# Kernel optimization log

Measured on AMD Instinct MI355X. Metric: run time of the kernel, lower is better.

The kernel has to match this reference:

```python
import jax, jax.numpy as jnp
import numpy as np

N_NODES, N_EDGES, N_GRAPHS = 500000, 2000000, 16384


def _lin(key, fan_in, fan_out):
    # torch nn.Linear default init: U(-1/sqrt(fan_in), 1/sqrt(fan_in))
    s = 1.0 / np.sqrt(fan_in)
    kw, kb = jax.random.split(key)
    W = jax.random.uniform(kw, (fan_in, fan_out), jnp.float32, -s, s)
    b = jax.random.uniform(kb, (fan_out,), jnp.float32, -s, s)
    return W, b


def setup_inputs() -> dict:
    key = jax.random.key(0)
    ks = jax.random.split(key, 16)
    x = jax.random.normal(ks[0], (N_NODES, 131), jnp.float32)
    edge_src = jax.random.randint(ks[1], (N_EDGES,), 0, N_NODES, jnp.int32)
    edge_dst = jax.random.randint(ks[2], (N_EDGES,), 0, N_NODES, jnp.int32)
    batch_index = jnp.sort(jax.random.randint(ks[3], (N_NODES,), 0, N_GRAPHS, jnp.int32))
    solvent_descriptors = jax.random.normal(ks[4], (N_GRAPHS, 11), jnp.float32)
    Wc1, bc1 = _lin(ks[5], 131, 128)
    Wc2, bc2 = _lin(ks[6], 128, 64)
    W1, b1 = _lin(ks[7], 64 + 11, 2048)
    W2, b2 = _lin(ks[8], 2048, 1024)
    W3, b3 = _lin(ks[9], 1024, 128)
    # 6 property heads, stacked: Linear(128,32) -> ReLU -> Linear(32,1)
    Wh1 = jnp.stack([_lin(jax.random.fold_in(ks[10], i), 128, 32)[0] for i in range(6)])
    bh1 = jnp.stack([_lin(jax.random.fold_in(ks[10], i), 128, 32)[1] for i in range(6)])
    Wh2 = jnp.stack([_lin(jax.random.fold_in(ks[11], i), 32, 1)[0] for i in range(6)])
    bh2 = jnp.stack([_lin(jax.random.fold_in(ks[11], i), 32, 1)[1] for i in range(6)])
    return dict(x=x, edge_src=edge_src, edge_dst=edge_dst, batch_index=batch_index,
                solvent_descriptors=solvent_descriptors,
                Wc1=Wc1, bc1=bc1, Wc2=Wc2, bc2=bc2,
                W1=W1, b1=b1, W2=W2, b2=b2, W3=W3, b3=b3,
                Wh1=Wh1, bh1=bh1, Wh2=Wh2, bh2=bh2,
                num_graphs=N_GRAPHS)


def _gcn_conv(x, W, b, src, dst, n_nodes):
    # PyG GCNConv: add self-loops, symmetric normalization, scatter-add aggregate.
    h = x @ W                                           # [N, F_out]
    deg = jnp.zeros((n_nodes,), x.dtype).at[dst].add(1.0) + 1.0  # +1 for self-loop
    dinv = jax.lax.rsqrt(deg)                            # deg >= 1
    norm = dinv[src] * dinv[dst]                         # [E]
    agg = jnp.zeros_like(h).at[dst].add(norm[:, None] * h[src])
    agg = agg + h * (dinv * dinv)[:, None]               # self-loop contribution
    return agg + b


def reference(x, edge_src, edge_dst, batch_index, solvent_descriptors,
              Wc1, bc1, Wc2, bc2, W1, b1, W2, b2, W3, b3,
              Wh1, bh1, Wh2, bh2, num_graphs):
    n = x.shape[0]
    h = jax.nn.relu(_gcn_conv(x, Wc1, bc1, edge_src, edge_dst, n))
    h = _gcn_conv(h, Wc2, bc2, edge_src, edge_dst, n)
    g = jax.ops.segment_sum(h, batch_index, num_segments=num_graphs)  # global sum pool [G,64]
    z = jnp.concatenate([g, solvent_descriptors], axis=1)             # [G,75]
    z = jax.nn.relu(z @ W1 + b1)   # dropout is identity in eval
    z = jax.nn.relu(z @ W2 + b2)
    z = jax.nn.relu(z @ W3 + b3)   # [G,128]
    a = jax.nn.relu(jnp.einsum('gf,hfk->ghk', z, Wh1) + bh1)          # [G,6,32]
    out = jnp.einsum('ghk,hk->gh', a, Wh2[..., 0]) + bh2[:, 0]        # [G,6]
    return out
```

## Files before the change

kernel.cpp:

```cpp
#include <hip/hip_runtime.h>

#define N_NODES 500000
#define N_EDGES 2000000
#define N_GRAPHS 16384
#define STRIP 16

#define SCAN_ELEMS 2048
#define SCAN_NBLK ((N_NODES + SCAN_ELEMS - 1) / SCAN_ELEMS)

typedef short bf16x8 __attribute__((ext_vector_type(8)));
typedef float f32x4 __attribute__((ext_vector_type(4)));
typedef unsigned short u16x8 __attribute__((ext_vector_type(8)));

__device__ __forceinline__ unsigned short f2bf_rne(float x) {
    unsigned int b = __float_as_uint(x);
    unsigned int r = (b + 0x7fffu + ((b >> 16) & 1u)) >> 16;
    return (unsigned short)r;
}
__device__ __forceinline__ float bf2f(unsigned short h) {
    return __uint_as_float(((unsigned int)h) << 16);
}
__device__ __forceinline__ void split_bf(float v, unsigned short& hi, unsigned short& lo) {
    hi = f2bf_rne(v);
    lo = f2bf_rne(v - bf2f(hi));
}

__global__ __launch_bounds__(256) void k_zero_counts(int* counts) {
    int i = blockIdx.x * 256 + threadIdx.x;
    if (i < N_NODES) counts[i] = 0;
}
__global__ __launch_bounds__(256) void k_hist(const int* __restrict__ dst, int* __restrict__ counts) {
    int e = blockIdx.x * 256 + threadIdx.x;
    if (e < N_EDGES) atomicAdd(&counts[dst[e]], 1);
}
__global__ __launch_bounds__(256) void k_scan_reduce(const int* __restrict__ counts, int* __restrict__ bsum) {
    int b = blockIdx.x, t = threadIdx.x;
    int base_i = b * SCAN_ELEMS + t * 8;
    int s = 0;
    #pragma unroll
    for (int j = 0; j < 8; j++) { int i = base_i + j; if (i < N_NODES) s += counts[i]; }
    __shared__ int sh[256];
    sh[t] = s; __syncthreads();
    for (int off = 128; off > 0; off >>= 1) { if (t < off) sh[t] += sh[t + off]; __syncthreads(); }
    if (t == 0) bsum[b] = sh[0];
}
__global__ __launch_bounds__(256) void k_scan_bsum(const int* __restrict__ bsum, int* __restrict__ boff,
                                                   int* __restrict__ row_ptr) {
    __shared__ int sh[256];
    int t = threadIdx.x;
    int v = (t < SCAN_NBLK) ? bsum[t] : 0;
    sh[t] = v; __syncthreads();
    for (int off = 1; off < 256; off <<= 1) {
        int u = (t >= off) ? sh[t - off] : 0;
        __syncthreads();
        sh[t] += u; __syncthreads();
    }
    boff[t] = sh[t] - v;
    if (t == 255) row_ptr[N_NODES] = sh[255];
}
__global__ __launch_bounds__(256) void k_scan_final(const int* __restrict__ counts, const int* __restrict__ boff,
                                                    int* __restrict__ row_ptr, int* __restrict__ cursor,
                                                    float* __restrict__ dinv) {
    __shared__ int sh[256];
    int b = blockIdx.x, t = threadIdx.x;
    int base_i = b * SCAN_ELEMS + t * 8;
    int c[8]; int tsum = 0;
    #pragma unroll
    for (int j = 0; j < 8; j++) {
        int i = base_i + j;
        c[j] = (i < N_NODES) ? counts[i] : 0;
        tsum += c[j];
    }
    sh[t] = tsum; __syncthreads();
    for (int off = 1; off < 256; off <<= 1) {
        int u = (t >= off) ? sh[t - off] : 0;
        __syncthreads();
        sh[t] += u; __syncthreads();
    }
    int run = boff[b] + sh[t] - tsum;
    #pragma unroll
    for (int j = 0; j < 8; j++) {
        int i = base_i + j;
        if (i < N_NODES) {
            row_ptr[i] = run;
            cursor[i]  = run;
            dinv[i]    = rsqrtf((float)c[j] + 1.0f);
        }
        run += c[j];
    }
}
__global__ __launch_bounds__(256) void k_fill(const int* __restrict__ esrc, const int* __restrict__ edst,
                                              int* __restrict__ cursor, int* __restrict__ srcs) {
    int e = blockIdx.x * 256 + threadIdx.x;
    if (e >= N_EDGES) return;
    int d = edst[e];
    int pos = atomicAdd(&cursor[d], 1);
    srcs[pos] = esrc[e];
}
__global__ __launch_bounds__(256) void k_gstart(const int* __restrict__ batch, int* __restrict__ gstart) {
    int g = blockIdx.x * 256 + threadIdx.x;
    if (g > N_GRAPHS) return;
    if (g == N_GRAPHS) { gstart[g] = N_NODES; return; }
    int lo = 0, hi = N_NODES;
    while (lo < hi) { int mid = (lo + hi) >> 1; if (batch[mid] < g) lo = mid + 1; else hi = mid; }
    gstart[g] = lo;
}
__global__ __launch_bounds__(256) void k_zero_P(float* P) {
    int i = blockIdx.x * 256 + threadIdx.x;
    if (i < N_GRAPHS * 128) P[i] = 0.0f;
}

template<int KTOT>
__global__ __launch_bounds__(256) void k_gemm_conv1(const float* __restrict__ A,
                                                    const float* __restrict__ B,
                                                    unsigned short* __restrict__ C, int Mreal) {
    __shared__ float As[8][132];
    __shared__ float Bs[8][132];
    const int tid = threadIdx.x;
    const int bm = blockIdx.x;
    const int tr = (tid >> 4) << 3;
    const int tc = (tid & 15) << 3;
    float acc[8][8] = {};
    const int la_r = tid >> 1, la_c = (tid & 1) << 2;
    const int lb_r = tid >> 5, lb_c = (tid & 31) << 2;
    const int arow = min(bm * 128 + la_r, Mreal - 1);
    const float* Ap = A + (size_t)arow * KTOT + la_c;
    constexpr int KMAIN = (KTOT / 8) * 8;
    for (int k0 = 0; k0 < KMAIN; k0 += 8) {
        float4 a4 = *(const float4*)(Ap + k0);
        float4 b4 = *(const float4*)(B + (size_t)(k0 + lb_r) * 128 + lb_c);
        __syncthreads();
        As[la_c + 0][la_r] = a4.x;
        As[la_c + 1][la_r] = a4.y;
        As[la_c + 2][la_r] = a4.z;
        As[la_c + 3][la_r] = a4.w;
        *(float4*)&Bs[lb_r][lb_c] = b4;
        __syncthreads();
        #pragma unroll
        for (int k = 0; k < 8; k++) {
            float a[8], b[8];
            *(float4*)&a[0] = *(const float4*)&As[k][tr];
            *(float4*)&a[4] = *(const float4*)&As[k][tr + 4];
            *(float4*)&b[0] = *(const float4*)&Bs[k][tc];
            *(float4*)&b[4] = *(const float4*)&Bs[k][tc + 4];
            #pragma unroll
            for (int i = 0; i < 8; i++)
                #pragma unroll
                for (int j = 0; j < 8; j++)
                    acc[i][j] = fmaf(a[i], b[j], acc[i][j]);
        }
    }
    if (KTOT % 8 != 0) {
        constexpr int k0 = KMAIN;
        float av[4];
        #pragma unroll
        for (int j = 0; j < 4; j++) av[j] = (k0 + la_c + j < KTOT) ? Ap[k0 + j] : 0.0f;
        float4 b4 = {0.f, 0.f, 0.f, 0.f};
        if (k0 + lb_r < KTOT) b4 = *(const float4*)(B + (size_t)(k0 + lb_r) * 128 + lb_c);
        __syncthreads();
        As[la_c + 0][la_r] = av[0];
        As[la_c + 1][la_r] = av[1];
        As[la_c + 2][la_r] = av[2];
        As[la_c + 3][la_r] = av[3];
        *(float4*)&Bs[lb_r][lb_c] = b4;
        __syncthreads();
        #pragma unroll
        for (int k = 0; k < 8; k++) {
            float a[8], b[8];
            *(float4*)&a[0] = *(const float4*)&As[k][tr];
            *(float4*)&a[4] = *(const float4*)&As[k][tr + 4];
            *(float4*)&b[0] = *(const float4*)&Bs[k][tc];
            *(float4*)&b[4] = *(const float4*)&Bs[k][tc + 4];
            #pragma unroll
            for (int i = 0; i < 8; i++)
                #pragma unroll
                for (int j = 0; j < 8; j++)
                    acc[i][j] = fmaf(a[i], b[j], acc[i][j]);
        }
    }
    const int row0 = bm * 128 + tr;
    #pragma unroll
    for (int i = 0; i < 8; i++) {
        if (row0 + i < Mreal) {
            u16x8 o;
            #pragma unroll
            for (int j = 0; j < 8; j++) o[j] = f2bf_rne(acc[i][j]);
            *(u16x8*)(C + (size_t)(row0 + i) * 128 + tc) = o;
        }
    }
}

__global__ __launch_bounds__(256) void k_gather1(const unsigned short* __restrict__ h,
                                                 const float* __restrict__ dinv,
                                                 const float* __restrict__ bias,
                                                 const int* __restrict__ row_ptr, const int* __restrict__ srcs,
                                                 unsigned short* __restrict__ r1) {
    int g = blockIdx.x * 256 + threadIdx.x;
    int n = g >> 6, lane = g & 63;
    if (n >= N_NODES) return;
    float dn = dinv[n];
    int c = lane * 2;
    unsigned int hv = *(const unsigned int*)(h + (size_t)n * 128 + c);
    float s2 = dn * dn;
    float a0 = fmaf(s2, bf2f((unsigned short)(hv & 0xffffu)), bias[c]);
    float a1 = fmaf(s2, bf2f((unsigned short)(hv >> 16)), bias[c + 1]);
    int e0 = row_ptr[n], e1 = row_ptr[n + 1];
    int e = e0;
    for (; e + 2 <= e1; e += 2) {
        int sA = srcs[e], sB = srcs[e + 1];
        float nA = dinv[sA] * dn, nB = dinv[sB] * dn;
        unsigned int hA = *(const unsigned int*)(h + (size_t)sA * 128 + c);
        unsigned int hB = *(const unsigned int*)(h + (size_t)sB * 128 + c);
        a0 = fmaf(nA, bf2f((unsigned short)(hA & 0xffffu)), a0);
        a1 = fmaf(nA, bf2f((unsigned short)(hA >> 16)), a1);
        a0 = fmaf(nB, bf2f((unsigned short)(hB & 0xffffu)), a0);
        a1 = fmaf(nB, bf2f((unsigned short)(hB >> 16)), a1);
    }
    if (e < e1) {
        int sA = srcs[e];
        float nA = dinv[sA] * dn;
        unsigned int hA = *(const unsigned int*)(h + (size_t)sA * 128 + c);
        a0 = fmaf(nA, bf2f((unsigned short)(hA & 0xffffu)), a0);
        a1 = fmaf(nA, bf2f((unsigned short)(hA >> 16)), a1);
    }
    a0 = fmaxf(a0, 0.0f);
    a1 = fmaxf(a1, 0.0f);
    unsigned int o = (unsigned int)f2bf_rne(a0) | ((unsigned int)f2bf_rne(a1) << 16);
    *(unsigned int*)(r1 + (size_t)n * 128 + c) = o;
}

__global__ __launch_bounds__(256) void k_g2p(const unsigned short* __restrict__ r1,
                                             const float* __restrict__ dinv,
                                             const int* __restrict__ row_ptr, const int* __restrict__ srcs,
                                             const int* __restrict__ batch,
                                             float* __restrict__ P) {
    int gw = (blockIdx.x * 256 + threadIdx.x) >> 6;
    int lane = threadIdx.x & 63;
    if (gw >= N_NODES / STRIP) return;
    int n0 = gw * STRIP;
    int c = lane * 2;
    float a0 = 0.0f, a1 = 0.0f;
    int cur_g = batch[n0];
    for (int n = n0; n < n0 + STRIP; n++) {
        int bg = batch[n];
        if (bg != cur_g) {
            atomicAdd(&P[(size_t)cur_g * 128 + c], a0);
            atomicAdd(&P[(size_t)cur_g * 128 + c + 1], a1);
            a0 = a1 = 0.0f;
            cur_g = bg;
        }
        float dn = dinv[n];
        float s2 = dn * dn;
        unsigned int hv = *(const unsigned int*)(r1 + (size_t)n * 128 + c);
        a0 = fmaf(s2, bf2f((unsigned short)(hv & 0xffffu)), a0);
        a1 = fmaf(s2, bf2f((unsigned short)(hv >> 16)), a1);
        int e0 = row_ptr[n], e1 = row_ptr[n + 1];
        int e = e0;
        for (; e + 2 <= e1; e += 2) {
            int sA = srcs[e], sB = srcs[e + 1];
            float nA = dinv[sA] * dn, nB = dinv[sB] * dn;
            unsigned int hA = *(const unsigned int*)(r1 + (size_t)sA * 128 + c);
            unsigned int hB = *(const unsigned int*)(r1 + (size_t)sB * 128 + c);
            a0 = fmaf(nA, bf2f((unsigned short)(hA & 0xffffu)), a0);
            a1 = fmaf(nA, bf2f((unsigned short)(hA >> 16)), a1);
            a0 = fmaf(nB, bf2f((unsigned short)(hB & 0xffffu)), a0);
            a1 = fmaf(nB, bf2f((unsigned short)(hB >> 16)), a1);
        }
        if (e < e1) {
            int sA = srcs[e];
            float nA = dinv[sA] * dn;
            unsigned int hA = *(const unsigned int*)(r1 + (size_t)sA * 128 + c);
            a0 = fmaf(nA, bf2f((unsigned short)(hA & 0xffffu)), a0);
            a1 = fmaf(nA, bf2f((unsigned short)(hA >> 16)), a1);
        }
    }
    atomicAdd(&P[(size_t)cur_g * 128 + c], a0);
    atomicAdd(&P[(size_t)cur_g * 128 + c + 1], a1);
}

__global__ __launch_bounds__(128) void k_zg(const float* __restrict__ P, const int* __restrict__ gstart,
                                            const float* __restrict__ Wc2, const float* __restrict__ bc2,
                                            const float* __restrict__ solv, float* __restrict__ zpad) {
    int g = blockIdx.x; int c = threadIdx.x;
    if (c >= 80) return;
    float v = 0.0f;
    if (c < 64) {
        const float* pr = P + (size_t)g * 128;
        float s = 0.0f;
        #pragma unroll 8
        for (int k = 0; k < 128; k++) s = fmaf(pr[k], Wc2[k * 64 + c], s);
        v = s + (float)(gstart[g + 1] - gstart[g]) * bc2[c];
    } else if (c < 75) {
        v = solv[g * 11 + (c - 64)];
    }
    zpad[(size_t)g * 80 + c] = v;
}

__global__ __launch_bounds__(256) void k_w1pad(const float* __restrict__ W1, float* __restrict__ w1pad) {
    int i = blockIdx.x * 256 + threadIdx.x;
    if (i >= 80 * 2048) return;
    int r = i / 2048, c = i % 2048;
    w1pad[i] = (r < 75) ? W1[r * 2048 + c] : 0.0f;
}

__global__ __launch_bounds__(256) void k_whcat(const float* __restrict__ Wh1, float* __restrict__ whcat) {
    int i = blockIdx.x * 256 + threadIdx.x;
    if (i >= 128 * 256) return;
    int f = i / 256, c = i % 256;
    float v = 0.0f;
    if (c < 192) {
        int h = c / 32, k = c & 31;
        v = Wh1[h * 128 * 32 + f * 32 + k];
    }
    whcat[i] = v;
}
__global__ __launch_bounds__(256) void k_bh1pad(const float* __restrict__ bh1, float* __restrict__ bh1pad) {
    int i = threadIdx.x;
    bh1pad[i] = (i < 192) ? bh1[i] : 0.0f;
}

__global__ __launch_bounds__(256) void k_tsplit(const float* __restrict__ W, int R, int C,
                                                unsigned short* __restrict__ Th, unsigned short* __restrict__ Tl) {
    __shared__ float tile[64][65];
    int cb = blockIdx.x * 64, rb = blockIdx.y * 64;
    int tc = threadIdx.x & 63, tr4 = threadIdx.x >> 6;
    #pragma unroll 4
    for (int i = 0; i < 16; i++) {
        int r = tr4 + i * 4;
        tile[r][tc] = W[(size_t)(rb + r) * C + cb + tc];
    }
    __syncthreads();
    #pragma unroll 4
    for (int i = 0; i < 16; i++) {
        int r = tr4 + i * 4;
        float v = tile[tc][r];
        unsigned short hi, lo; split_bf(v, hi, lo);
        size_t o = (size_t)(cb + r) * R + rb + tc;
        Th[o] = hi; Tl[o] = lo;
    }
}

template<bool RELU, int OMODE>
__global__ __launch_bounds__(256) void k_gemm(const float* __restrict__ A,
                                              const float* __restrict__ B,
                                              const float* __restrict__ bias,
                                              float* __restrict__ C,
                                              unsigned short* __restrict__ Ch,
                                              unsigned short* __restrict__ Cl,
                                              int M, int N, int K) {
    __shared__ float As[8][132];
    __shared__ float Bs[8][132];
    const int tid = threadIdx.x;
    const int bm = blockIdx.y, bn = blockIdx.x;
    const int tr = (tid >> 4) << 3;
    const int tc = (tid & 15) << 3;
    float acc[8][8] = {};
    const float* Ab = A + (size_t)bm * 128 * K;
    const float* Bb = B + (size_t)bn * 128;
    const int la_r = tid >> 1, la_c = (tid & 1) << 2;
    const int lb_r = tid >> 5, lb_c = (tid & 31) << 2;
    for (int k0 = 0; k0 < K; k0 += 8) {
        float4 a4 = *(const float4*)(Ab + (size_t)la_r * K + k0 + la_c);
        float4 b4 = *(const float4*)(Bb + (size_t)(k0 + lb_r) * N + lb_c);
        __syncthreads();
        As[la_c + 0][la_r] = a4.x;
        As[la_c + 1][la_r] = a4.y;
        As[la_c + 2][la_r] = a4.z;
        As[la_c + 3][la_r] = a4.w;
        *(float4*)&Bs[lb_r][lb_c] = b4;
        __syncthreads();
        #pragma unroll
        for (int k = 0; k < 8; k++) {
            float a[8], b[8];
            *(float4*)&a[0] = *(const float4*)&As[k][tr];
            *(float4*)&a[4] = *(const float4*)&As[k][tr + 4];
            *(float4*)&b[0] = *(const float4*)&Bs[k][tc];
            *(float4*)&b[4] = *(const float4*)&Bs[k][tc + 4];
            #pragma unroll
            for (int i = 0; i < 8; i++)
                #pragma unroll
                for (int j = 0; j < 8; j++)
                    acc[i][j] = fmaf(a[i], b[j], acc[i][j]);
        }
    }
    const int row0 = bm * 128 + tr, col0 = bn * 128 + tc;
    #pragma unroll
    for (int i = 0; i < 8; i++) {
        if (OMODE == 0) {
            #pragma unroll
            for (int j = 0; j < 8; j++) {
                float v = acc[i][j] + bias[col0 + j];
                if (RELU) v = fmaxf(v, 0.0f);
                acc[i][j] = v;
            }
            *(float4*)(C + (size_t)(row0 + i) * N + col0)     = *(float4*)&acc[i][0];
            *(float4*)(C + (size_t)(row0 + i) * N + col0 + 4) = *(float4*)&acc[i][4];
        } else {
            u16x8 h8, l8;
            #pragma unroll
            for (int j = 0; j < 8; j++) {
                float v = acc[i][j] + bias[col0 + j];
                if (RELU) v = fmaxf(v, 0.0f);
                unsigned short hi, lo; split_bf(v, hi, lo);
                h8[j] = hi; l8[j] = lo;
            }
            *(u16x8*)(Ch + (size_t)(row0 + i) * N + col0) = h8;
            *(u16x8*)(Cl + (size_t)(row0 + i) * N + col0) = l8;
        }
    }
}

template<int OMODE>
__global__ __launch_bounds__(256) void k_mfma_split(
        const unsigned short* __restrict__ Ah, const unsigned short* __restrict__ Al,
        const unsigned short* __restrict__ Bh, const unsigned short* __restrict__ Bl,
        const float* __restrict__ bias,
        float* __restrict__ C, unsigned short* __restrict__ Ch, unsigned short* __restrict__ Cl,
        int N, int K) {
    __shared__ short lds[32768];
    const int tid = threadIdx.x;
    const int w = tid >> 6, l = tid & 63;
    const int id = blockIdx.x;
    const int bm = id & 127;
    const int bn = id >> 7;
    const unsigned short* gmat = (w == 0) ? Ah : (w == 1) ? Al : (w == 2) ? Bh : Bl;
    const size_t grow0 = (size_t)((w < 2) ? bm : bn) * 128 + (l >> 3);
    const int koffg = ((l & 7) ^ ((l >> 3) & 7)) * 8;
    const int ldsw = w * 8192;
    const int wm = w >> 1, wn = w & 1;
    const int lane15 = l & 15, lg = l >> 4, l7 = l & 7;
    f32x4 acc[4][4] = {};
    const int NK = K >> 6;
    for (int kt = 0; kt < NK; kt++) {
        const int k0 = kt << 6;
        __syncthreads();
        #pragma unroll
        for (int i = 0; i < 16; i++) {
            const unsigned short* src = gmat + (grow0 + (size_t)i * 8) * (size_t)K + k0 + koffg;
            __builtin_amdgcn_global_load_lds(
                (const __attribute__((address_space(1))) unsigned int*)src,
                (__attribute__((address_space(3))) unsigned int*)&lds[ldsw + i * 512],
                16, 0, 0);
        }
        __syncthreads();
        #pragma unroll
        for (int kh = 0; kh < 2; kh++) {
            const int slot = ((kh * 4 + lg) ^ l7) * 8;
            bf16x8 ahf[4], alf[4], bhf[4], blf[4];
            #pragma unroll
            for (int m = 0; m < 4; m++) {
                int si = (wm * 64 + m * 16 + lane15) * 64 + slot;
                ahf[m] = *(const bf16x8*)&lds[si];
                alf[m] = *(const bf16x8*)&lds[8192 + si];
            }
            #pragma unroll
            for (int n = 0; n < 4; n++) {
                int si = (wn * 64 + n * 16 + lane15) * 64 + slot;
                bhf[n] = *(const bf16x8*)&lds[16384 + si];
                blf[n] = *(const bf16x8*)&lds[24576 + si];
            }
            #pragma unroll
            for (int m = 0; m < 4; m++)
                #pragma unroll
                for (int n = 0; n < 4; n++) {
                    acc[m][n] = __builtin_amdgcn_mfma_f32_16x16x32_bf16(ahf[m], bhf[n], acc[m][n], 0, 0, 0);
                    acc[m][n] = __builtin_amdgcn_mfma_f32_16x16x32_bf16(ahf[m], blf[n], acc[m][n], 0, 0, 0);
                    acc[m][n] = __builtin_amdgcn_mfma_f32_16x16x32_bf16(alf[m], bhf[n], acc[m][n], 0, 0, 0);
                }
        }
    }
    const int row_b = bm * 128 + wm * 64 + lg * 4;
    const int col_b = bn * 128 + wn * 64 + lane15;
    #pragma unroll
    for (int m = 0; m < 4; m++)
        #pragma unroll
        for (int n = 0; n < 4; n++) {
            int col = col_b + n * 16;
            float bv = bias[col];
            #pragma unroll
            for (int j = 0; j < 4; j++) {
                int row = row_b + m * 16 + j;
                float v = fmaxf(acc[m][n][j] + bv, 0.0f);
                size_t o = (size_t)row * N + col;
                if (OMODE == 0) {
                    C[o] = v;
                } else {
                    unsigned short hi, lo; split_bf(v, hi, lo);
                    Ch[o] = hi; Cl[o] = lo;
                }
            }
        }
}

__global__ __launch_bounds__(256) void k_heads_out(const float* __restrict__ a,
                                                   const float* __restrict__ Wh2,
                                                   const float* __restrict__ bh2,
                                                   float* __restrict__ out) {
    int i = blockIdx.x * 256 + threadIdx.x;
    if (i >= N_GRAPHS * 6) return;
    int g = i / 6, h = i % 6;
    const float* ap = a + (size_t)g * 256 + h * 32;
    const float* wp = Wh2 + h * 32;
    float s = 0.0f;
    #pragma unroll
    for (int k = 0; k < 32; k++) s = fmaf(ap[k], wp[k], s);
    out[i] = s + bh2[h];
}

extern "C" void kernel_launch(void* const* d_in, const int* in_sizes, int n_in,
                              void* d_out, int out_size, void* d_ws, size_t ws_size,
                              hipStream_t stream) {
    const float* x    = (const float*)d_in[0];
    const int*   esrc = (const int*)d_in[1];
    const int*   edst = (const int*)d_in[2];
    const int*   batch= (const int*)d_in[3];
    const float* solv = (const float*)d_in[4];
    const float* Wc1  = (const float*)d_in[5];
    const float* bc1  = (const float*)d_in[6];
    const float* Wc2  = (const float*)d_in[7];
    const float* bc2  = (const float*)d_in[8];
    const float* W1   = (const float*)d_in[9];
    const float* b1   = (const float*)d_in[10];
    const float* W2   = (const float*)d_in[11];
    const float* b2   = (const float*)d_in[12];
    const float* W3   = (const float*)d_in[13];
    const float* b3   = (const float*)d_in[14];
    const float* Wh1  = (const float*)d_in[15];
    const float* bh1  = (const float*)d_in[16];
    const float* Wh2  = (const float*)d_in[17];
    const float* bh2  = (const float*)d_in[18];
    float* out = (float*)d_out;

    float* ws    = (float*)d_ws;
    float* bufA  = ws;
    float* bufB  = bufA + 64000000;
    float* dinv  = bufB + 64000000;
    float* zpad  = dinv + 524288;
    float* w1pad = zpad + (size_t)N_GRAPHS * 80;
    float* whcat = w1pad + 80 * 2048;
    float* bh1p  = whcat + 128 * 256;
    int* counts  = (int*)(bh1p + 256);
    int* row_ptr = counts + N_NODES;
    int* cursor  = row_ptr + 500224;
    int* srcs    = cursor + N_NODES;
    int* bsum    = srcs + N_EDGES;
    int* boff    = bsum + 256;
    int* gstart  = boff + 256;
    float* P     = bufB + 61902848;

    unsigned short* h_bf = (unsigned short*)bufA;
    unsigned short* r1   = (unsigned short*)bufB;

    unsigned short* z1h = (unsigned short*)bufB;
    unsigned short* z1l = (unsigned short*)(bufB + 16800000);
    unsigned short* z2h = (unsigned short*)bufA;
    unsigned short* z2l = (unsigned short*)(bufA + 8400000);
    float* z3 = bufB + 34000000;
    unsigned short* w2th = (unsigned short*)(bufA + 33000000);
    unsigned short* w2tl = (unsigned short*)(bufA + 34100000);
    unsigned short* w3th = (unsigned short*)(bufA + 35200000);
    unsigned short* w3tl = (unsigned short*)(bufA + 35300000);
    float* ab = bufA + 36000000;

    k_zero_counts<<<(N_NODES + 255) / 256, 256, 0, stream>>>(counts);
    k_hist<<<(N_EDGES + 255) / 256, 256, 0, stream>>>(edst, counts);
    k_scan_reduce<<<SCAN_NBLK, 256, 0, stream>>>(counts, bsum);
    k_scan_bsum<<<1, 256, 0, stream>>>(bsum, boff, row_ptr);
    k_scan_final<<<SCAN_NBLK, 256, 0, stream>>>(counts, boff, row_ptr, cursor, dinv);
    k_fill<<<(N_EDGES + 255) / 256, 256, 0, stream>>>(esrc, edst, cursor, srcs);
    k_gstart<<<(N_GRAPHS + 256) / 256, 256, 0, stream>>>(batch, gstart);
    k_zero_P<<<(N_GRAPHS * 128) / 256, 256, 0, stream>>>(P);

    k_gemm_conv1<131><<<(N_NODES + 127) / 128, 256, 0, stream>>>(x, Wc1, h_bf, N_NODES);
    k_gather1<<<(N_NODES * 64) / 256, 256, 0, stream>>>(h_bf, dinv, bc1, row_ptr, srcs, r1);

    k_g2p<<<((N_NODES / STRIP) * 64 + 255) / 256, 256, 0, stream>>>(r1, dinv, row_ptr, srcs, batch, P);

    k_tsplit<<<dim3(1024 / 64, 2048 / 64), 256, 0, stream>>>(W2, 2048, 1024, w2th, w2tl);
    k_tsplit<<<dim3(128 / 64, 1024 / 64), 256, 0, stream>>>(W3, 1024, 128, w3th, w3tl);

    k_zg<<<N_GRAPHS, 128, 0, stream>>>(P, gstart, Wc2, bc2, solv, zpad);

    k_w1pad<<<(80 * 2048) / 256, 256, 0, stream>>>(W1, w1pad);
    k_whcat<<<(128 * 256) / 256, 256, 0, stream>>>(Wh1, whcat);
    k_bh1pad<<<1, 256, 0, stream>>>(bh1, bh1p);

    k_gemm<true, 1><<<dim3(2048 / 128, N_GRAPHS / 128), 256, 0, stream>>>(
        zpad, w1pad, b1, nullptr, z1h, z1l, N_GRAPHS, 2048, 80);
    k_mfma_split<1><<<(1024 / 128) * (N_GRAPHS / 128), 256, 0, stream>>>(
        z1h, z1l, w2th, w2tl, b2, nullptr, z2h, z2l, 1024, 2048);
    k_mfma_split<0><<<(128 / 128) * (N_GRAPHS / 128), 256, 0, stream>>>(
        z2h, z2l, w3th, w3tl, b3, z3, nullptr, nullptr, 128, 1024);

    k_gemm<true, 0><<<dim3(256 / 128, N_GRAPHS / 128), 256, 0, stream>>>(
        z3, whcat, bh1p, ab, nullptr, nullptr, N_GRAPHS, 256, 128);
    k_heads_out<<<(N_GRAPHS * 6 + 255) / 256, 256, 0, stream>>>(ab, Wh2, bh2, out);
}
```

Measured before the change: 1.251 ms.

## Replace FP32 conv1 GEMM with bf16 MFMA using padded bf16 input

Converts the node features x into a padded bf16 matrix (K padded to 192) and splits Wc1 into hi/lo bf16 parts. The first GCN linear layer then runs on 16x16x32 bf16 MFMA instructions, with async global-to-LDS loads and swizzled LDS, in place of the scalar FP32 FMA tile GEMM. The goal is to cut the compute cost of the 500k x 131 x 128 GEMM. In exchange it adds an extra pass that reads x and writes a bf16 copy. It also drops x's low-order bits, since only the weights get the hi/lo split, so accuracy is lower than before.

```diff
diff --git a/kernel.cpp b/kernel.cpp
--- a/kernel.cpp
+++ b/kernel.cpp
@@ -4,6 +4,8 @@
 #define N_EDGES 2000000
 #define N_GRAPHS 16384
 #define STRIP 16
+#define MPAD 500096
+#define KC1 192
 
 #define SCAN_ELEMS 2048
 #define SCAN_NBLK ((N_NODES + SCAN_ELEMS - 1) / SCAN_ELEMS)
@@ -110,84 +112,106 @@
     if (i < N_GRAPHS * 128) P[i] = 0.0f;
 }
 
-template<int KTOT>
-__global__ __launch_bounds__(256) void k_gemm_conv1(const float* __restrict__ A,
-                                                    const float* __restrict__ B,
-                                                    unsigned short* __restrict__ C, int Mreal) {
-    __shared__ float As[8][132];
-    __shared__ float Bs[8][132];
+__global__ __launch_bounds__(256) void k_xsplit(const float* __restrict__ x, unsigned short* __restrict__ xb) {
+    int idx = blockIdx.x * 256 + threadIdx.x;
+    if (idx >= MPAD * (KC1 / 8)) return;
+    int n = idx / (KC1 / 8);
+    int c8 = (idx % (KC1 / 8)) * 8;
+    u16x8 o;
+    #pragma unroll
+    for (int j = 0; j < 8; j++) {
+        int k = c8 + j;
+        float v = (k < 131 && n < N_NODES) ? x[(size_t)n * 131 + k] : 0.0f;
+        o[j] = f2bf_rne(v);
+    }
+    *(u16x8*)(xb + (size_t)n * KC1 + c8) = o;
+}
+
+__global__ __launch_bounds__(256) void k_wc1split(const float* __restrict__ W,
+                                                  unsigned short* __restrict__ Th,
+                                                  unsigned short* __restrict__ Tl) {
+    int idx = blockIdx.x * 256 + threadIdx.x;
+    if (idx >= 128 * KC1) return;
+    int c = idx / KC1, k = idx % KC1;
+    float v = (k < 131) ? W[(size_t)k * 128 + c] : 0.0f;
+    unsigned short hi, lo; split_bf(v, hi, lo);
+    Th[idx] = hi; Tl[idx] = lo;
+}
+
+__global__ __launch_bounds__(256) void k_mfma_conv1(const unsigned short* __restrict__ Abf,
+                                                    const unsigned short* __restrict__ Bh,
+                                                    const unsigned short* __restrict__ Bl,
+                                                    unsigned short* __restrict__ C) {
+    __shared__ short lds[24576];
     const int tid = threadIdx.x;
+    const int w = tid >> 6, l = tid & 63;
     const int bm = blockIdx.x;
-    const int tr = (tid >> 4) << 3;
-    const int tc = (tid & 15) << 3;
-    float acc[8][8] = {};
-    const int la_r = tid >> 1, la_c = (tid & 1) << 2;
-    const int lb_r = tid >> 5, lb_c = (tid & 31) << 2;
-    const int arow = min(bm * 128 + la_r, Mreal - 1);
-    const float* Ap = A + (size_t)arow * KTOT + la_c;
-    constexpr int KMAIN = (KTOT / 8) * 8;
-    for (int k0 = 0; k0 < KMAIN; k0 += 8) {
-        float4 a4 = *(const float4*)(Ap + k0);
-        float4 b4 = *(const float4*)(B + (size_t)(k0 + lb_r) * 128 + lb_c);
-        __syncthreads();
-        As[la_c + 0][la_r] = a4.x;
-        As[la_c + 1][la_r] = a4.y;
-        As[la_c + 2][la_r] = a4.z;
-        As[la_c + 3][la_r] = a4.w;
-        *(float4*)&Bs[lb_r][lb_c] = b4;
+    const int wm = w >> 1, wn = w & 1;
+    const int lane15 = l & 15, lg = l >> 4, l7 = l & 7;
+    const int koffg = ((l & 7) ^ ((l >> 3) & 7)) * 8;
+    f32x4 acc[4][4] = {};
+    for (int kt = 0; kt < 3; kt++) {
+        const int k0 = kt * 64;
+        __syncthreads();
+        if (w < 2) {
+            #pragma unroll
+            for (int i = 0; i < 8; i++) {
+                size_t row = (size_t)bm * 128 + w * 64 + i * 8 + (l >> 3);
+                const unsigned short* src = Abf + row * KC1 + k0 + koffg;
+                __builtin_amdgcn_global_load_lds(
+                    (const __attribute__((address_space(1))) unsigned int*)src,
+                    (__attribute__((address_space(3))) unsigned int*)&lds[w * 4096 + i * 512],
+                    16, 0, 0);
+            }
+        } else {
+            const unsigned short* gB = (w == 2) ? Bh : Bl;
+            #pragma unroll
+            for (int i = 0; i < 16; i++) {
+                int row = i * 8 + (l >> 3);
+                const unsigned short* src = gB + (size_t)row * KC1 + k0 + koffg;
+                __builtin_amdgcn_global_load_lds(
+                    (const __attribute__((address_space(1))) unsigned int*)src,
+                    (__attribute__((address_space(3))) unsigned int*)&lds[(w - 1) * 8192 + i * 512],
+                    16, 0, 0);
+            }
+        }
         __syncthreads();
         #pragma unroll
-        for (int k = 0; k < 8; k++) {
-            float a[8], b[8];
-            *(float4*)&a[0] = *(const float4*)&As[k][tr];
-            *(float4*)&a[4] = *(const float4*)&As[k][tr + 4];
-            *(float4*)&b[0] = *(const float4*)&Bs[k][tc];
-            *(float4*)&b[4] = *(const float4*)&Bs[k][tc + 4];
-            #pragma unroll
-            for (int i = 0; i < 8; i++)
+        for (int kh = 0; kh < 2; kh++) {
+            const int slot = ((kh * 4 + lg) ^ l7) * 8;
+            bf16x8 af[4], bhf[4], blf[4];
+            #pragma unroll
+            for (int m = 0; m < 4; m++)
+                af[m] = *(const bf16x8*)&lds[(wm * 64 + m * 16 + lane15) * 64 + slot];
+            #pragma unroll
+            for (int n = 0; n < 4; n++) {
+                int si = (wn * 64 + n * 16 + lane15) * 64 + slot;
+                bhf[n] = *(const bf16x8*)&lds[8192 + si];
+                blf[n] = *(const bf16x8*)&lds[16384 + si];
+            }
+            #pragma unroll
+            for (int m = 0; m < 4; m++)
                 #pragma unroll
-                for (int j = 0; j < 8; j++)
-                    acc[i][j] = fmaf(a[i], b[j], acc[i][j]);
-        }
-    }
-    if (KTOT % 8 != 0) {
-        constexpr int k0 = KMAIN;
-        float av[4];
+                for (int n = 0; n < 4; n++) {
+                    acc[m][n] = __builtin_amdgcn_mfma_f32_16x16x32_bf16(af[m], bhf[n], acc[m][n], 0, 0, 0);
+                    acc[m][n] = __builtin_amdgcn_mfma_f32_16x16x32_bf16(af[m], blf[n], acc[m][n], 0, 0, 0);
+                }
+        }
+    }
+    const size_t row_b = (size_t)bm * 128 + wm * 64 + lg * 4;
+    const int col_b = wn * 64 + lane15;
+    #pragma unroll
+    for (int m = 0; m < 4; m++)
         #pragma unroll
-        for (int j = 0; j < 4; j++) av[j] = (k0 + la_c + j < KTOT) ? Ap[k0 + j] : 0.0f;
-        float4 b4 = {0.f, 0.f, 0.f, 0.f};
-        if (k0 + lb_r < KTOT) b4 = *(const float4*)(B + (size_t)(k0 + lb_r) * 128 + lb_c);
-        __syncthreads();
-        As[la_c + 0][la_r] = av[0];
-        As[la_c + 1][la_r] = av[1];
-        As[la_c + 2][la_r] = av[2];
-        As[la_c + 3][la_r] = av[3];
-        *(float4*)&Bs[lb_r][lb_c] = b4;
-        __syncthreads();
-        #pragma unroll
-        for (int k = 0; k < 8; k++) {
-            float a[8], b[8];
-            *(float4*)&a[0] = *(const float4*)&As[k][tr];
-            *(float4*)&a[4] = *(const float4*)&As[k][tr + 4];
-            *(float4*)&b[0] = *(const float4*)&Bs[k][tc];
-            *(float4*)&b[4] = *(const float4*)&Bs[k][tc + 4];
-            #pragma unroll
-            for (int i = 0; i < 8; i++)
-                #pragma unroll
-                for (int j = 0; j < 8; j++)
-                    acc[i][j] = fmaf(a[i], b[j], acc[i][j]);
-        }
-    }
-    const int row0 = bm * 128 + tr;
-    #pragma unroll
-    for (int i = 0; i < 8; i++) {
-        if (row0 + i < Mreal) {
-            u16x8 o;
-            #pragma unroll
-            for (int j = 0; j < 8; j++) o[j] = f2bf_rne(acc[i][j]);
-            *(u16x8*)(C + (size_t)(row0 + i) * 128 + tc) = o;
-        }
-    }
+        for (int n = 0; n < 4; n++) {
+            int col = col_b + n * 16;
+            #pragma unroll
+            for (int j = 0; j < 4; j++) {
+                size_t row = row_b + m * 16 + j;
+                if (row < N_NODES)
+                    C[row * 128 + col] = f2bf_rne(acc[m][n][j]);
+            }
+        }
 }
 
 __global__ __launch_bounds__(256) void k_gather1(const unsigned short* __restrict__ h,
@@ -549,7 +573,10 @@
     float* P     = bufB + 61902848;
 
     unsigned short* h_bf = (unsigned short*)bufA;
+    unsigned short* x_bf = (unsigned short*)bufB;
     unsigned short* r1   = (unsigned short*)bufB;
+    unsigned short* wc1h = (unsigned short*)(bufA + 60000000);
+    unsigned short* wc1l = wc1h + 128 * KC1;
 
     unsigned short* z1h = (unsigned short*)bufB;
     unsigned short* z1l = (unsigned short*)(bufB + 16800000);
@@ -571,7 +598,10 @@
     k_gstart<<<(N_GRAPHS + 256) / 256, 256, 0, stream>>>(batch, gstart);
     k_zero_P<<<(N_GRAPHS * 128) / 256, 256, 0, stream>>>(P);
 
-    k_gemm_conv1<131><<<(N_NODES + 127) / 128, 256, 0, stream>>>(x, Wc1, h_bf, N_NODES);
+    k_xsplit<<<(MPAD * (KC1 / 8) + 255) / 256, 256, 0, stream>>>(x, x_bf);
+    k_wc1split<<<(128 * KC1 + 255) / 256, 256, 0, stream>>>(Wc1, wc1h, wc1l);
+    k_mfma_conv1<<<MPAD / 128, 256, 0, stream>>>(x_bf, wc1h, wc1l, h_bf);
+
     k_gather1<<<(N_NODES * 64) / 256, 256, 0, stream>>>(h_bf, dinv, bc1, row_ptr, srcs, r1);
 
     k_g2p<<<((N_NODES / STRIP) * 64 + 255) / 256, 256, 0, stream>>>(r1, dinv, row_ptr, srcs, batch, P);
```

Measured after the change: 1.224 ms. -2.2%, faster.
